# Performance work log

Measured on AMD Instinct MI355X. Metric: run time of the kernel, lower is better.

The kernel has to match this reference:

```python
import jax, jax.numpy as jnp
import numpy as np

EPS = 1e-5  # torch.nn.LayerNorm default
NUM_HEADS = 8


def _layernorm(x, g, b):
    mu = jnp.mean(x, axis=-1, keepdims=True)
    var = jnp.mean((x - mu) ** 2, axis=-1, keepdims=True)
    return (x - mu) * jax.lax.rsqrt(var + EPS) * g + b


def setup_inputs() -> dict:
    key = jax.random.key(0)
    ks = jax.random.split(key, 8)
    B, S, D = 4, 2048, 512
    scale = 0.02
    return {
        'x': jax.random.normal(ks[0], (B, S, D), dtype=jnp.float32),
        'gene_types': jax.random.randint(ks[1], (B, S), 0, 2),
        'tf_g': jnp.ones((D,), jnp.float32), 'tf_b': jnp.zeros((D,), jnp.float32),
        'tg_g': jnp.ones((D,), jnp.float32), 'tg_b': jnp.zeros((D,), jnp.float32),
        'in_proj_w': jax.random.normal(ks[2], (3 * D, D), dtype=jnp.float32) * scale,
        'in_proj_b': jnp.zeros((3 * D,), jnp.float32),
        'out_proj_w': jax.random.normal(ks[3], (D, D), dtype=jnp.float32) * scale,
        'out_proj_b': jnp.zeros((D,), jnp.float32),
        'w1': jax.random.normal(ks[4], (D // 2, D), dtype=jnp.float32) * scale,
        'b1': jnp.zeros((D // 2,), jnp.float32),
        'w2': jax.random.normal(ks[5], (1, D // 2), dtype=jnp.float32) * scale,
        'b2': jnp.zeros((1,), jnp.float32),
    }


def reference(x, gene_types, tf_g, tf_b, tg_g, tg_b,
              in_proj_w, in_proj_b, out_proj_w, out_proj_b,
              w1, b1, w2, b2):
    B, S, D = x.shape
    H = NUM_HEADS
    HD = D // H
    # --- vectorized per-token conditional LayerNorm (gene_type 0 -> tf, 1 -> target, else passthrough) ---
    gt = gene_types[..., None]
    xn = jnp.where(gt == 0, _layernorm(x, tf_g, tf_b),
                   jnp.where(gt == 1, _layernorm(x, tg_g, tg_b), x))
    # --- multi-head self-attention (torch MultiheadAttention, batch_first) ---
    qkv = xn @ in_proj_w.T + in_proj_b            # [B,S,3D]
    q, k, v = jnp.split(qkv, 3, axis=-1)
    to_heads = lambda t: t.reshape(B, S, H, HD).transpose(0, 2, 1, 3)  # [B,H,S,HD]
    q, k, v = to_heads(q), to_heads(k), to_heads(v)
    scores = jnp.einsum('bhqd,bhkd->bhqk', q, k) / jnp.sqrt(jnp.float32(HD))
    attn = jax.nn.softmax(scores, axis=-1)
    o = jnp.einsum('bhqk,bhkd->bhqd', attn, v)
    o = o.transpose(0, 2, 1, 3).reshape(B, S, D)
    o = o @ out_proj_w.T + out_proj_b
    xr = xn + o                                    # residual
    # --- regulatory strength gate: Linear -> SiLU -> Linear -> Sigmoid ---
    h = jax.nn.silu(xr @ w1.T + b1)                # [B,S,D/2]
    strength = jax.nn.sigmoid(h @ w2.T + b2)       # [B,S,1]
    return xr * strength
```

## Files before the change

kernel.cpp:

```cpp
#include <hip/hip_runtime.h>

typedef __bf16 bf16;
typedef __bf16 bf16x4_t __attribute__((ext_vector_type(4)));
typedef __bf16 bf16x8_t __attribute__((ext_vector_type(8)));
typedef float f32x4_t __attribute__((ext_vector_type(4)));

#define MFMA16(a, b, c) __builtin_amdgcn_mfma_f32_16x16x32_bf16(a, b, c, 0, 0, 0)

__global__ void cast3_k(const float* __restrict__ a, const float* __restrict__ b,
                        const float* __restrict__ c, bf16* __restrict__ da,
                        bf16* __restrict__ db, bf16* __restrict__ dc) {
    int i = blockIdx.x * blockDim.x + threadIdx.x;
    if (i < 786432) da[i] = (bf16)a[i];
    else if (i < 1048576) db[i - 786432] = (bf16)b[i - 786432];
    else if (i < 1179648) dc[i - 1048576] = (bf16)c[i - 1048576];
}

__global__ __launch_bounds__(256) void ln_k(const float* __restrict__ x,
                                            const int* __restrict__ gt,
                                            const float* __restrict__ tfg,
                                            const float* __restrict__ tfb,
                                            const float* __restrict__ tgg,
                                            const float* __restrict__ tgb,
                                            bf16* __restrict__ xn) {
    int t = blockIdx.x;
    int tid = threadIdx.x;
    const float* xr = x + (size_t)t * 512;
    float2 v = ((const float2*)xr)[tid];
    float s = v.x + v.y;
    float sq = v.x * v.x + v.y * v.y;
    for (int m = 1; m < 64; m <<= 1) {
        s += __shfl_xor(s, m, 64);
        sq += __shfl_xor(sq, m, 64);
    }
    __shared__ float ss[4], ssq[4];
    if ((tid & 63) == 0) { ss[tid >> 6] = s; ssq[tid >> 6] = sq; }
    __syncthreads();
    s = ss[0] + ss[1] + ss[2] + ss[3];
    sq = ssq[0] + ssq[1] + ssq[2] + ssq[3];
    float mean = s * (1.f / 512.f);
    float var = fmaxf(sq * (1.f / 512.f) - mean * mean, 0.f);
    float rstd = rsqrtf(var + 1e-5f);
    int g = gt[t];
    int d0 = tid * 2;
    float o0, o1;
    if (g == 0) {
        o0 = (v.x - mean) * rstd * tfg[d0] + tfb[d0];
        o1 = (v.y - mean) * rstd * tfg[d0 + 1] + tfb[d0 + 1];
    } else if (g == 1) {
        o0 = (v.x - mean) * rstd * tgg[d0] + tgb[d0];
        o1 = (v.y - mean) * rstd * tgg[d0 + 1] + tgb[d0 + 1];
    } else {
        o0 = v.x; o1 = v.y;
    }
    bf16* xo = xn + (size_t)t * 512 + d0;
    xo[0] = (bf16)o0;
    xo[1] = (bf16)o1;
}

template <int EPI>
__global__ __launch_bounds__(256) void gemm_k(const bf16* __restrict__ A,
                                              const bf16* __restrict__ B,
                                              const float* __restrict__ bias,
                                              bf16* __restrict__ p0,
                                              bf16* __restrict__ p1,
                                              bf16* __restrict__ p2,
                                              const bf16* __restrict__ xn,
                                              float* __restrict__ xrf) {
    int m0 = blockIdx.x * 128, n0 = blockIdx.y * 128;
    int tid = threadIdx.x;
    int lane = tid & 63, w = tid >> 6;
    int quad = lane >> 4, l15 = lane & 15;
    int wm = (w >> 1) * 64, wn = (w & 1) * 64;
    __shared__ bf16 As[128 * 72];
    __shared__ bf16 Bs[128 * 72];
    f32x4_t acc[4][4] = {};
    int srow = tid >> 3, ssub = tid & 7;
    const bf16* Ab = A + (size_t)(m0 + srow) * 512 + ssub * 8;
    const bf16* Bb = B + (size_t)(n0 + srow) * 512 + ssub * 8;
    uint4 pa[4], pb[4];
    auto gload = [&](int s) {
        int k0 = s * 64;
#pragma unroll
        for (int i = 0; i < 4; ++i) {
            pa[i] = *(const uint4*)(Ab + (size_t)(i * 32) * 512 + k0);
            pb[i] = *(const uint4*)(Bb + (size_t)(i * 32) * 512 + k0);
        }
    };
    auto sstore = [&]() {
#pragma unroll
        for (int i = 0; i < 4; ++i) {
            *(uint4*)&As[(i * 32 + srow) * 72 + ssub * 8] = pa[i];
            *(uint4*)&Bs[(i * 32 + srow) * 72 + ssub * 8] = pb[i];
        }
    };
    gload(0);
    sstore();
    for (int s = 0; s < 8; ++s) {
        __syncthreads();
        if (s < 7) gload(s + 1);
#pragma unroll
        for (int ks = 0; ks < 2; ++ks) {
            bf16x8_t af[4], bfr[4];
            int koff = ks * 32 + quad * 8;
#pragma unroll
            for (int mt = 0; mt < 4; ++mt)
                af[mt] = *(const bf16x8_t*)&As[(wm + mt * 16 + l15) * 72 + koff];
#pragma unroll
            for (int nt = 0; nt < 4; ++nt)
                bfr[nt] = *(const bf16x8_t*)&Bs[(wn + nt * 16 + l15) * 72 + koff];
#pragma unroll
            for (int mt = 0; mt < 4; ++mt)
#pragma unroll
                for (int nt = 0; nt < 4; ++nt)
                    acc[mt][nt] = MFMA16(af[mt], bfr[nt], acc[mt][nt]);
        }
        __syncthreads();
        if (s < 7) sstore();
    }
#pragma unroll
    for (int mt = 0; mt < 4; ++mt) {
#pragma unroll
        for (int nt = 0; nt < 4; ++nt) {
            int gcol = n0 + wn + nt * 16 + l15;
            float bcol = bias[gcol];
#pragma unroll
            for (int r = 0; r < 4; ++r) {
                int grow = m0 + wm + mt * 16 + quad * 4 + r;
                float v = acc[mt][nt][r] + bcol;
                if constexpr (EPI == 0) {
                    int which = gcol >> 9;
                    int d = gcol & 511;
                    int hh = d >> 6, hd = d & 63;
                    int b = grow >> 11, ssi = grow & 2047;
                    size_t bh = (size_t)(b * 8 + hh);
                    if (which == 0) {
                        p0[(bh * 2048 + ssi) * 64 + hd] = (bf16)(v * 0.180336880111f);
                    } else if (which == 1) {
                        p1[(bh * 2048 + ssi) * 64 + hd] = (bf16)v;
                    } else {
                        p2[(bh * 64 + hd) * 2048 + ssi] = (bf16)v;
                    }
                } else if constexpr (EPI == 1) {
                    size_t idx = (size_t)grow * 512 + gcol;
                    float xv = v + (float)xn[idx];
                    xrf[idx] = xv;
                    p0[idx] = (bf16)xv;
                } else {
                    float sv = v / (1.f + __expf(-v));
                    p0[(size_t)grow * 256 + gcol] = (bf16)sv;
                }
            }
        }
    }
    (void)p1; (void)p2; (void)xn; (void)xrf;
}

__global__ __launch_bounds__(256) void attn_k(const bf16* __restrict__ q,
                                              const bf16* __restrict__ k,
                                              const bf16* __restrict__ vt,
                                              bf16* __restrict__ pO,
                                              float* __restrict__ pL) {
    int bh = blockIdx.y;
    int q0 = blockIdx.x * 128;
    int sz = blockIdx.z;
    int tid = threadIdx.x;
    int lane = tid & 63, w = tid >> 6;
    int quad = lane >> 4, l15 = lane & 15;
    __shared__ bf16 Ks[64 * 72];
    __shared__ bf16 Vs[64 * 72];
    __shared__ bf16 Ps[128 * 72];
    const bf16* qb = q + (size_t)bh * 2048 * 64;
    const bf16* kb = k + (size_t)bh * 2048 * 64;
    const bf16* vb = vt + (size_t)bh * 64 * 2048;
    bf16x8_t qf[2][2];
#pragma unroll
    for (int mt = 0; mt < 2; ++mt)
#pragma unroll
        for (int ks = 0; ks < 2; ++ks)
            qf[mt][ks] = *(const bf16x8_t*)(qb + (size_t)(q0 + w * 32 + mt * 16 + l15) * 64 + ks * 32 + quad * 8);
    bf16x8_t ones;
#pragma unroll
    for (int i = 0; i < 8; ++i) ones[i] = (bf16)1.0f;
    f32x4_t oacc[2][4] = {};
    f32x4_t lacc[2] = {};
    int srow = tid >> 3, ssub = tid & 7;
    for (int kt = sz * 16; kt < sz * 16 + 16; ++kt) {
        int kbase = kt * 64;
        __syncthreads();
#pragma unroll
        for (int i = 0; i < 2; ++i) {
            int row = i * 32 + srow;
            *(uint4*)&Ks[row * 72 + ssub * 8] = *(const uint4*)(kb + (size_t)(kbase + row) * 64 + ssub * 8);
            *(uint4*)&Vs[row * 72 + ssub * 8] = *(const uint4*)(vb + (size_t)row * 2048 + kbase + ssub * 8);
        }
        __syncthreads();
        f32x4_t sacc[2][4] = {};
#pragma unroll
        for (int ks = 0; ks < 2; ++ks) {
            bf16x8_t kf[4];
            int koff = ks * 32 + quad * 8;
#pragma unroll
            for (int nt = 0; nt < 4; ++nt) kf[nt] = *(const bf16x8_t*)&Ks[(nt * 16 + l15) * 72 + koff];
#pragma unroll
            for (int mt = 0; mt < 2; ++mt)
#pragma unroll
                for (int nt = 0; nt < 4; ++nt)
                    sacc[mt][nt] = MFMA16(qf[mt][ks], kf[nt], sacc[mt][nt]);
        }
#pragma unroll
        for (int mt = 0; mt < 2; ++mt)
#pragma unroll
            for (int nt = 0; nt < 4; ++nt)
#pragma unroll
                for (int r = 0; r < 4; ++r)
                    Ps[(w * 32 + mt * 16 + quad * 4 + r) * 72 + nt * 16 + l15] = (bf16)exp2f(sacc[mt][nt][r]);
#pragma unroll
        for (int ks = 0; ks < 2; ++ks) {
            int koff = ks * 32 + quad * 8;
            bf16x8_t pf[2], vf[4];
#pragma unroll
            for (int mt = 0; mt < 2; ++mt) pf[mt] = *(const bf16x8_t*)&Ps[(w * 32 + mt * 16 + l15) * 72 + koff];
#pragma unroll
            for (int nt = 0; nt < 4; ++nt) vf[nt] = *(const bf16x8_t*)&Vs[(nt * 16 + l15) * 72 + koff];
#pragma unroll
            for (int mt = 0; mt < 2; ++mt) {
#pragma unroll
                for (int nt = 0; nt < 4; ++nt)
                    oacc[mt][nt] = MFMA16(pf[mt], vf[nt], oacc[mt][nt]);
                lacc[mt] = MFMA16(pf[mt], ones, lacc[mt]);
            }
        }
    }
    size_t obase = ((size_t)(sz * 32 + bh) * 2048 + q0);
#pragma unroll
    for (int mt = 0; mt < 2; ++mt)
#pragma unroll
        for (int r = 0; r < 4; ++r) {
            int row = w * 32 + mt * 16 + quad * 4 + r;
#pragma unroll
            for (int nt = 0; nt < 4; ++nt)
                pO[(obase + row) * 64 + nt * 16 + l15] = (bf16)oacc[mt][nt][r];
            if (l15 == 0) pL[obase + row] = lacc[mt][r];
        }
}

__global__ __launch_bounds__(256) void comb_k(const bf16* __restrict__ pO,
                                              const float* __restrict__ pL,
                                              bf16* __restrict__ o) {
    int i = blockIdx.x * 256 + threadIdx.x;
    int hd = (i & 15) * 4;
    int s = (i >> 4) & 2047;
    int bh = i >> 15;
    size_t r0 = (size_t)bh * 2048 + s;
    size_t r1 = (size_t)(32 + bh) * 2048 + s;
    float inv = 1.f / (pL[r0] + pL[r1]);
    bf16x4_t a = *(const bf16x4_t*)(pO + r0 * 64 + hd);
    bf16x4_t b = *(const bf16x4_t*)(pO + r1 * 64 + hd);
    int bb = bh >> 3, hh = bh & 7;
    bf16x4_t ov;
#pragma unroll
    for (int j = 0; j < 4; ++j) ov[j] = (bf16)(((float)a[j] + (float)b[j]) * inv);
    *(bf16x4_t*)(o + ((size_t)(bb * 2048 + s) * 512) + hh * 64 + hd) = ov;
}

__global__ __launch_bounds__(256) void gate_k(const bf16* __restrict__ h,
                                              const float* __restrict__ w2,
                                              const float* __restrict__ b2,
                                              const float* __restrict__ xrf,
                                              float* __restrict__ out) {
    int t = blockIdx.x * 4 + (threadIdx.x >> 6);
    int lane = threadIdx.x & 63;
    const bf16* hr = h + (size_t)t * 256;
    bf16x4_t hv = *(const bf16x4_t*)(hr + lane * 4);
    float4 wv = *(const float4*)(w2 + lane * 4);
    float dot = (float)hv[0] * wv.x + (float)hv[1] * wv.y + (float)hv[2] * wv.z + (float)hv[3] * wv.w;
    for (int m = 1; m < 64; m <<= 1) dot += __shfl_xor(dot, m, 64);
    float st = 1.f / (1.f + __expf(-(dot + b2[0])));
    const float4* x4 = (const float4*)(xrf + (size_t)t * 512);
    float4* o4 = (float4*)(out + (size_t)t * 512);
#pragma unroll
    for (int j = 0; j < 2; ++j) {
        float4 xv = x4[lane * 2 + j];
        float4 ov;
        ov.x = xv.x * st; ov.y = xv.y * st; ov.z = xv.z * st; ov.w = xv.w * st;
        o4[lane * 2 + j] = ov;
    }
}

extern "C" void kernel_launch(void* const* d_in, const int* in_sizes, int n_in,
                              void* d_out, int out_size, void* d_ws, size_t ws_size,
                              hipStream_t stream) {
    const float* x    = (const float*)d_in[0];
    const int*   gt   = (const int*)d_in[1];
    const float* tfg  = (const float*)d_in[2];
    const float* tfb  = (const float*)d_in[3];
    const float* tgg  = (const float*)d_in[4];
    const float* tgb  = (const float*)d_in[5];
    const float* Wqkv = (const float*)d_in[6];
    const float* bqkv = (const float*)d_in[7];
    const float* Wout = (const float*)d_in[8];
    const float* bout = (const float*)d_in[9];
    const float* W1   = (const float*)d_in[10];
    const float* b1   = (const float*)d_in[11];
    const float* w2   = (const float*)d_in[12];
    const float* b2   = (const float*)d_in[13];
    float* out = (float*)d_out;
    char* ws = (char*)d_ws;

    const size_t MB = 1024 * 1024;
    bf16*  xn  = (bf16*)(ws + 0);
    bf16*  q   = (bf16*)(ws + 8 * MB);
    bf16*  o   = (bf16*)(ws + 8 * MB);
    bf16*  kk  = (bf16*)(ws + 16 * MB);
    bf16*  vt  = (bf16*)(ws + 24 * MB);
    float* xrf = (float*)(ws + 16 * MB);
    bf16*  pO  = (bf16*)(ws + 32 * MB);
    bf16*  xrb = (bf16*)(ws + 32 * MB);
    bf16*  h   = (bf16*)(ws + 40 * MB);
    bf16*  wq  = (bf16*)(ws + 48 * MB);
    bf16*  wo  = (bf16*)(ws + 48 * MB + 1536 * 512 * 2);
    bf16*  w1b = (bf16*)(ws + 48 * MB + (1536 + 512) * 512 * 2);
    float* pL  = (float*)(ws + 48 * MB + 2304 * 512 * 2);

    cast3_k<<<4608, 256, 0, stream>>>(Wqkv, Wout, W1, wq, wo, w1b);
    ln_k<<<8192, 256, 0, stream>>>(x, gt, tfg, tfb, tgg, tgb, xn);
    gemm_k<0><<<dim3(64, 12), 256, 0, stream>>>(xn, wq, bqkv, q, kk, vt, nullptr, nullptr);
    attn_k<<<dim3(16, 32, 2), 256, 0, stream>>>(q, kk, vt, pO, pL);
    comb_k<<<4096, 256, 0, stream>>>(pO, pL, o);
    gemm_k<1><<<dim3(64, 4), 256, 0, stream>>>(o, wo, bout, xrb, nullptr, nullptr, xn, xrf);
    gemm_k<2><<<dim3(64, 2), 256, 0, stream>>>(xrb, w1b, b1, h, nullptr, nullptr, nullptr, nullptr);
    gate_k<<<2048, 256, 0, stream>>>(h, w2, b2, xrf, out);
    (void)in_sizes; (void)n_in; (void)out_size; (void)ws_size;
}
```

Measured before the change: 342.5 us.

## Keep P in registers, prefetch K/V tiles, vectorize layernorm, allow 4-way key split

The attention kernel now computes S transposed (K times Q) so the exponentiated scores already sit in the register layout a 16x16x16 MFMA needs. P stays in registers and the shared-memory round trip and the Ps buffer are dropped. K/V tiles are loaded from global into registers one iteration ahead of their store to LDS. The key-dimension split becomes a parameter, set to 4 when the workspace is large enough, and the combine kernel loops over the splits. Layernorm now gives each wavefront one row with float4 loads and no LDS reduction, and the workspace buffers are reordered. The narrower K=16 MFMA and the extra partial outputs may cost throughput and memory traffic.

```diff
diff --git a/kernel.cpp b/kernel.cpp
--- a/kernel.cpp
+++ b/kernel.cpp
@@ -6,6 +6,19 @@
 typedef float f32x4_t __attribute__((ext_vector_type(4)));
 
 #define MFMA16(a, b, c) __builtin_amdgcn_mfma_f32_16x16x32_bf16(a, b, c, 0, 0, 0)
+
+static __device__ __forceinline__ f32x4_t mfma_k16(bf16x4_t a, bf16x4_t b, f32x4_t c) {
+#if __has_builtin(__builtin_amdgcn_mfma_f32_16x16x16bf16_1k)
+    typedef short s16x4_t __attribute__((ext_vector_type(4)));
+    return __builtin_amdgcn_mfma_f32_16x16x16bf16_1k(
+        __builtin_bit_cast(s16x4_t, a), __builtin_bit_cast(s16x4_t, b), c, 0, 0, 0);
+#else
+    bf16x8_t az = {}, bz = {};
+    az[0] = a[0]; az[1] = a[1]; az[2] = a[2]; az[3] = a[3];
+    bz[0] = b[0]; bz[1] = b[1]; bz[2] = b[2]; bz[3] = b[3];
+    return MFMA16(az, bz, c);
+#endif
+}
 
 __global__ void cast3_k(const float* __restrict__ a, const float* __restrict__ b,
                         const float* __restrict__ c, bf16* __restrict__ da,
@@ -23,39 +36,44 @@
                                             const float* __restrict__ tgg,
                                             const float* __restrict__ tgb,
                                             bf16* __restrict__ xn) {
-    int t = blockIdx.x;
-    int tid = threadIdx.x;
-    const float* xr = x + (size_t)t * 512;
-    float2 v = ((const float2*)xr)[tid];
-    float s = v.x + v.y;
-    float sq = v.x * v.x + v.y * v.y;
+    int wid = threadIdx.x >> 6, lane = threadIdx.x & 63;
+    int t = blockIdx.x * 4 + wid;
+    const float4* xr = (const float4*)(x + (size_t)t * 512);
+    float4 a = xr[lane * 2], b = xr[lane * 2 + 1];
+    float s = (a.x + a.y) + (a.z + a.w) + (b.x + b.y) + (b.z + b.w);
+    float sq = a.x * a.x + a.y * a.y + a.z * a.z + a.w * a.w +
+               b.x * b.x + b.y * b.y + b.z * b.z + b.w * b.w;
     for (int m = 1; m < 64; m <<= 1) {
         s += __shfl_xor(s, m, 64);
         sq += __shfl_xor(sq, m, 64);
     }
-    __shared__ float ss[4], ssq[4];
-    if ((tid & 63) == 0) { ss[tid >> 6] = s; ssq[tid >> 6] = sq; }
-    __syncthreads();
-    s = ss[0] + ss[1] + ss[2] + ss[3];
-    sq = ssq[0] + ssq[1] + ssq[2] + ssq[3];
     float mean = s * (1.f / 512.f);
     float var = fmaxf(sq * (1.f / 512.f) - mean * mean, 0.f);
     float rstd = rsqrtf(var + 1e-5f);
     int g = gt[t];
-    int d0 = tid * 2;
-    float o0, o1;
-    if (g == 0) {
-        o0 = (v.x - mean) * rstd * tfg[d0] + tfb[d0];
-        o1 = (v.y - mean) * rstd * tfg[d0 + 1] + tfb[d0 + 1];
-    } else if (g == 1) {
-        o0 = (v.x - mean) * rstd * tgg[d0] + tgb[d0];
-        o1 = (v.y - mean) * rstd * tgg[d0 + 1] + tgb[d0 + 1];
+    float4 o0, o1;
+    if (g < 2) {
+        const float4* gp = (const float4*)(g ? tgg : tfg);
+        const float4* bp = (const float4*)(g ? tgb : tfb);
+        float4 g0 = gp[lane * 2], g1 = gp[lane * 2 + 1];
+        float4 b0 = bp[lane * 2], b1 = bp[lane * 2 + 1];
+        o0.x = (a.x - mean) * rstd * g0.x + b0.x;
+        o0.y = (a.y - mean) * rstd * g0.y + b0.y;
+        o0.z = (a.z - mean) * rstd * g0.z + b0.z;
+        o0.w = (a.w - mean) * rstd * g0.w + b0.w;
+        o1.x = (b.x - mean) * rstd * g1.x + b1.x;
+        o1.y = (b.y - mean) * rstd * g1.y + b1.y;
+        o1.z = (b.z - mean) * rstd * g1.z + b1.z;
+        o1.w = (b.w - mean) * rstd * g1.w + b1.w;
     } else {
-        o0 = v.x; o1 = v.y;
-    }
-    bf16* xo = xn + (size_t)t * 512 + d0;
-    xo[0] = (bf16)o0;
-    xo[1] = (bf16)o1;
+        o0 = a; o1 = b;
+    }
+    bf16* xo = xn + (size_t)t * 512 + lane * 8;
+    bf16x4_t p0, p1;
+    p0[0] = (bf16)o0.x; p0[1] = (bf16)o0.y; p0[2] = (bf16)o0.z; p0[3] = (bf16)o0.w;
+    p1[0] = (bf16)o1.x; p1[1] = (bf16)o1.y; p1[2] = (bf16)o1.z; p1[3] = (bf16)o1.w;
+    *(bf16x4_t*)xo = p0;
+    *(bf16x4_t*)(xo + 4) = p1;
 }
 
 template <int EPI>
@@ -160,107 +178,128 @@
                                               const bf16* __restrict__ k,
                                               const bf16* __restrict__ vt,
                                               bf16* __restrict__ pO,
-                                              float* __restrict__ pL) {
+                                              float* __restrict__ pL,
+                                              int nsplit) {
     int bh = blockIdx.y;
     int q0 = blockIdx.x * 128;
     int sz = blockIdx.z;
+    int tiles = 32 / nsplit;
+    int kt0 = sz * tiles;
     int tid = threadIdx.x;
     int lane = tid & 63, w = tid >> 6;
     int quad = lane >> 4, l15 = lane & 15;
     __shared__ bf16 Ks[64 * 72];
     __shared__ bf16 Vs[64 * 72];
-    __shared__ bf16 Ps[128 * 72];
     const bf16* qb = q + (size_t)bh * 2048 * 64;
     const bf16* kb = k + (size_t)bh * 2048 * 64;
     const bf16* vb = vt + (size_t)bh * 64 * 2048;
     bf16x8_t qf[2][2];
 #pragma unroll
-    for (int mt = 0; mt < 2; ++mt)
+    for (int qt = 0; qt < 2; ++qt)
 #pragma unroll
         for (int ks = 0; ks < 2; ++ks)
-            qf[mt][ks] = *(const bf16x8_t*)(qb + (size_t)(q0 + w * 32 + mt * 16 + l15) * 64 + ks * 32 + quad * 8);
-    bf16x8_t ones;
-#pragma unroll
-    for (int i = 0; i < 8; ++i) ones[i] = (bf16)1.0f;
+            qf[qt][ks] = *(const bf16x8_t*)(qb + (size_t)(q0 + w * 32 + qt * 16 + l15) * 64 + ks * 32 + quad * 8);
+    bf16x4_t ones4;
+#pragma unroll
+    for (int i = 0; i < 4; ++i) ones4[i] = (bf16)1.0f;
     f32x4_t oacc[2][4] = {};
     f32x4_t lacc[2] = {};
     int srow = tid >> 3, ssub = tid & 7;
-    for (int kt = sz * 16; kt < sz * 16 + 16; ++kt) {
+    uint4 pk[2], pv[2];
+    auto gload = [&](int kt) {
         int kbase = kt * 64;
-        __syncthreads();
 #pragma unroll
         for (int i = 0; i < 2; ++i) {
             int row = i * 32 + srow;
-            *(uint4*)&Ks[row * 72 + ssub * 8] = *(const uint4*)(kb + (size_t)(kbase + row) * 64 + ssub * 8);
-            *(uint4*)&Vs[row * 72 + ssub * 8] = *(const uint4*)(vb + (size_t)row * 2048 + kbase + ssub * 8);
-        }
+            pk[i] = *(const uint4*)(kb + (size_t)(kbase + row) * 64 + ssub * 8);
+            pv[i] = *(const uint4*)(vb + (size_t)row * 2048 + kbase + ssub * 8);
+        }
+    };
+    auto sstore = [&]() {
+#pragma unroll
+        for (int i = 0; i < 2; ++i) {
+            int row = i * 32 + srow;
+            *(uint4*)&Ks[row * 72 + ssub * 8] = pk[i];
+            *(uint4*)&Vs[row * 72 + ssub * 8] = pv[i];
+        }
+    };
+    gload(kt0);
+    for (int kt = kt0; kt < kt0 + tiles; ++kt) {
         __syncthreads();
-        f32x4_t sacc[2][4] = {};
-#pragma unroll
-        for (int ks = 0; ks < 2; ++ks) {
-            bf16x8_t kf[4];
-            int koff = ks * 32 + quad * 8;
-#pragma unroll
-            for (int nt = 0; nt < 4; ++nt) kf[nt] = *(const bf16x8_t*)&Ks[(nt * 16 + l15) * 72 + koff];
-#pragma unroll
-            for (int mt = 0; mt < 2; ++mt)
-#pragma unroll
-                for (int nt = 0; nt < 4; ++nt)
-                    sacc[mt][nt] = MFMA16(qf[mt][ks], kf[nt], sacc[mt][nt]);
-        }
-#pragma unroll
-        for (int mt = 0; mt < 2; ++mt)
-#pragma unroll
-            for (int nt = 0; nt < 4; ++nt)
-#pragma unroll
-                for (int r = 0; r < 4; ++r)
-                    Ps[(w * 32 + mt * 16 + quad * 4 + r) * 72 + nt * 16 + l15] = (bf16)exp2f(sacc[mt][nt][r]);
+        sstore();
+        __syncthreads();
+        if (kt + 1 < kt0 + tiles) gload(kt + 1);
+        f32x4_t sacc[4][2] = {};
 #pragma unroll
         for (int ks = 0; ks < 2; ++ks) {
             int koff = ks * 32 + quad * 8;
-            bf16x8_t pf[2], vf[4];
-#pragma unroll
-            for (int mt = 0; mt < 2; ++mt) pf[mt] = *(const bf16x8_t*)&Ps[(w * 32 + mt * 16 + l15) * 72 + koff];
-#pragma unroll
-            for (int nt = 0; nt < 4; ++nt) vf[nt] = *(const bf16x8_t*)&Vs[(nt * 16 + l15) * 72 + koff];
-#pragma unroll
-            for (int mt = 0; mt < 2; ++mt) {
-#pragma unroll
-                for (int nt = 0; nt < 4; ++nt)
-                    oacc[mt][nt] = MFMA16(pf[mt], vf[nt], oacc[mt][nt]);
-                lacc[mt] = MFMA16(pf[mt], ones, lacc[mt]);
+            bf16x8_t kf[4];
+#pragma unroll
+            for (int nt = 0; nt < 4; ++nt)
+                kf[nt] = *(const bf16x8_t*)&Ks[(nt * 16 + l15) * 72 + koff];
+#pragma unroll
+            for (int nt = 0; nt < 4; ++nt)
+#pragma unroll
+                for (int qt = 0; qt < 2; ++qt)
+                    sacc[nt][qt] = MFMA16(kf[nt], qf[qt][ks], sacc[nt][qt]);
+        }
+        bf16x4_t pf[4][2];
+#pragma unroll
+        for (int nt = 0; nt < 4; ++nt)
+#pragma unroll
+            for (int qt = 0; qt < 2; ++qt)
+#pragma unroll
+                for (int r = 0; r < 4; ++r)
+                    pf[nt][qt][r] = (bf16)exp2f(sacc[nt][qt][r]);
+#pragma unroll
+        for (int nt = 0; nt < 4; ++nt) {
+            bf16x4_t vf[4];
+#pragma unroll
+            for (int dt = 0; dt < 4; ++dt)
+                vf[dt] = *(const bf16x4_t*)&Vs[(dt * 16 + l15) * 72 + nt * 16 + quad * 4];
+#pragma unroll
+            for (int qt = 0; qt < 2; ++qt) {
+#pragma unroll
+                for (int dt = 0; dt < 4; ++dt)
+                    oacc[qt][dt] = mfma_k16(pf[nt][qt], vf[dt], oacc[qt][dt]);
+                lacc[qt] = mfma_k16(pf[nt][qt], ones4, lacc[qt]);
             }
         }
     }
     size_t obase = ((size_t)(sz * 32 + bh) * 2048 + q0);
 #pragma unroll
-    for (int mt = 0; mt < 2; ++mt)
+    for (int qt = 0; qt < 2; ++qt)
 #pragma unroll
         for (int r = 0; r < 4; ++r) {
-            int row = w * 32 + mt * 16 + quad * 4 + r;
-#pragma unroll
-            for (int nt = 0; nt < 4; ++nt)
-                pO[(obase + row) * 64 + nt * 16 + l15] = (bf16)oacc[mt][nt][r];
-            if (l15 == 0) pL[obase + row] = lacc[mt][r];
+            int row = w * 32 + qt * 16 + quad * 4 + r;
+#pragma unroll
+            for (int dt = 0; dt < 4; ++dt)
+                pO[(obase + row) * 64 + dt * 16 + l15] = (bf16)oacc[qt][dt][r];
+            if (l15 == 0) pL[obase + row] = lacc[qt][r];
         }
 }
 
 __global__ __launch_bounds__(256) void comb_k(const bf16* __restrict__ pO,
                                               const float* __restrict__ pL,
-                                              bf16* __restrict__ o) {
+                                              bf16* __restrict__ o, int nsplit) {
     int i = blockIdx.x * 256 + threadIdx.x;
     int hd = (i & 15) * 4;
     int s = (i >> 4) & 2047;
     int bh = i >> 15;
-    size_t r0 = (size_t)bh * 2048 + s;
-    size_t r1 = (size_t)(32 + bh) * 2048 + s;
-    float inv = 1.f / (pL[r0] + pL[r1]);
-    bf16x4_t a = *(const bf16x4_t*)(pO + r0 * 64 + hd);
-    bf16x4_t b = *(const bf16x4_t*)(pO + r1 * 64 + hd);
+    float l = 0.f;
+    float acc[4] = {};
+    for (int sp = 0; sp < nsplit; ++sp) {
+        size_t r = (size_t)(sp * 32 + bh) * 2048 + s;
+        l += pL[r];
+        bf16x4_t a = *(const bf16x4_t*)(pO + r * 64 + hd);
+#pragma unroll
+        for (int j = 0; j < 4; ++j) acc[j] += (float)a[j];
+    }
+    float inv = 1.f / l;
     int bb = bh >> 3, hh = bh & 7;
     bf16x4_t ov;
 #pragma unroll
-    for (int j = 0; j < 4; ++j) ov[j] = (bf16)(((float)a[j] + (float)b[j]) * inv);
+    for (int j = 0; j < 4; ++j) ov[j] = (bf16)(acc[j] * inv);
     *(bf16x4_t*)(o + ((size_t)(bb * 2048 + s) * 512) + hh * 64 + hd) = ov;
 }
 
@@ -309,27 +348,29 @@
     char* ws = (char*)d_ws;
 
     const size_t MB = 1024 * 1024;
-    bf16*  xn  = (bf16*)(ws + 0);
-    bf16*  q   = (bf16*)(ws + 8 * MB);
-    bf16*  o   = (bf16*)(ws + 8 * MB);
-    bf16*  kk  = (bf16*)(ws + 16 * MB);
-    bf16*  vt  = (bf16*)(ws + 24 * MB);
-    float* xrf = (float*)(ws + 16 * MB);
-    bf16*  pO  = (bf16*)(ws + 32 * MB);
-    bf16*  xrb = (bf16*)(ws + 32 * MB);
-    bf16*  h   = (bf16*)(ws + 40 * MB);
-    bf16*  wq  = (bf16*)(ws + 48 * MB);
-    bf16*  wo  = (bf16*)(ws + 48 * MB + 1536 * 512 * 2);
-    bf16*  w1b = (bf16*)(ws + 48 * MB + (1536 + 512) * 512 * 2);
-    float* pL  = (float*)(ws + 48 * MB + 2304 * 512 * 2);
+    bf16*  wq  = (bf16*)(ws + 0);
+    bf16*  wo  = (bf16*)(ws + 1536 * 512 * 2);
+    bf16*  w1b = (bf16*)(ws + (1536 + 512) * 512 * 2);
+    float* pL  = (float*)(ws + 2304 * 512 * 2);
+    bf16*  xn  = (bf16*)(ws + 4 * MB);
+    bf16*  q   = (bf16*)(ws + 12 * MB);
+    bf16*  o   = (bf16*)(ws + 12 * MB);
+    bf16*  kk  = (bf16*)(ws + 20 * MB);
+    bf16*  vt  = (bf16*)(ws + 28 * MB);
+    float* xrf = (float*)(ws + 20 * MB);
+    bf16*  pO  = (bf16*)(ws + 36 * MB);
+    bf16*  xrb = (bf16*)(ws + 36 * MB);
+    bf16*  h   = (bf16*)(ws + 44 * MB);
+
+    int nsplit = (ws_size >= 69 * MB) ? 4 : 2;
 
     cast3_k<<<4608, 256, 0, stream>>>(Wqkv, Wout, W1, wq, wo, w1b);
-    ln_k<<<8192, 256, 0, stream>>>(x, gt, tfg, tfb, tgg, tgb, xn);
+    ln_k<<<2048, 256, 0, stream>>>(x, gt, tfg, tfb, tgg, tgb, xn);
     gemm_k<0><<<dim3(64, 12), 256, 0, stream>>>(xn, wq, bqkv, q, kk, vt, nullptr, nullptr);
-    attn_k<<<dim3(16, 32, 2), 256, 0, stream>>>(q, kk, vt, pO, pL);
-    comb_k<<<4096, 256, 0, stream>>>(pO, pL, o);
+    attn_k<<<dim3(16, 32, nsplit), 256, 0, stream>>>(q, kk, vt, pO, pL, nsplit);
+    comb_k<<<4096, 256, 0, stream>>>(pO, pL, o, nsplit);
     gemm_k<1><<<dim3(64, 4), 256, 0, stream>>>(o, wo, bout, xrb, nullptr, nullptr, xn, xrf);
     gemm_k<2><<<dim3(64, 2), 256, 0, stream>>>(xrb, w1b, b1, h, nullptr, nullptr, nullptr, nullptr);
     gate_k<<<2048, 256, 0, stream>>>(h, w2, b2, xrf, out);
-    (void)in_sizes; (void)n_in; (void)out_size; (void)ws_size;
-}
+    (void)in_sizes; (void)n_in; (void)out_size;
+}
```

After: 345.0 us. About the same (+0.7%).
